# Kernel optimization log

Measured on AMD Instinct MI355X. Metric: run time of the kernel, lower is better.

## Reference

```python
import jax, jax.numpy as jnp
import numpy as np

NEG_SLOPE = 0.2


def _gat_layer(x, src, dst, W, att_src, att_dst, bias, concat):
    # x: [N, F_in]; W: [F_in, H*C]; att_*: [H, C]; bias: [H*C] or [C]
    N = x.shape[0]
    H, C = att_src.shape
    h = (x @ W).reshape(N, H, C)                      # [N, H, C]
    a_src = jnp.einsum('nhc,hc->nh', h, att_src)      # [N, H]
    a_dst = jnp.einsum('nhc,hc->nh', h, att_dst)      # [N, H]
    e = jax.nn.leaky_relu(a_src[src] + a_dst[dst], NEG_SLOPE)  # [E, H]
    # segment softmax over incoming edges of each destination node
    m = jax.ops.segment_max(e, dst, num_segments=N)   # [N, H]
    ex = jnp.exp(e - m[dst])
    s = jax.ops.segment_sum(ex, dst, num_segments=N)  # [N, H]
    alpha = ex / s[dst]                               # [E, H]
    out = jax.ops.segment_sum(h[src] * alpha[:, :, None], dst, num_segments=N)  # [N,H,C]
    out = out.reshape(N, H * C) if concat else out.mean(axis=1)
    return out + bias


def setup_inputs() -> dict:
    key = jax.random.key(0)
    ks = jax.random.split(key, 16)
    N, E, F = 50000, 1600000, 128
    HC1, H1 = 32, 4
    HC2, H2 = 32, 2
    NC, H3 = 2, 1     # layer3: 64 -> 2, 1 head, concat=False
    g = lambda k, shape, scale: jax.random.normal(k, shape, dtype=jnp.float32) * scale
    return {
        'x': g(ks[0], (N, F), 1.0),
        'edge_index': jax.random.randint(ks[1], (2, E), 0, N, dtype=jnp.int32),
        'W1': g(ks[2], (F, H1 * HC1), 0.1),
        'as1': g(ks[3], (H1, HC1), 0.1),
        'ad1': g(ks[4], (H1, HC1), 0.1),
        'b1': jnp.zeros((H1 * HC1,), jnp.float32),
        'W2': g(ks[5], (H1 * HC1, H2 * HC2), 0.1),
        'as2': g(ks[6], (H2, HC2), 0.1),
        'ad2': g(ks[7], (H2, HC2), 0.1),
        'b2': jnp.zeros((H2 * HC2,), jnp.float32),
        'W3': g(ks[8], (H2 * HC2, H3 * NC), 0.1),
        'as3': g(ks[9], (H3, NC), 0.1),
        'ad3': g(ks[10], (H3, NC), 0.1),
        'b3': jnp.zeros((NC,), jnp.float32),
    }


def reference(x, edge_index, W1, as1, ad1, b1, W2, as2, ad2, b2, W3, as3, ad3, b3):
    N = x.shape[0]
    # PyG GATConv adds self-loops by default
    loops = jnp.arange(N, dtype=edge_index.dtype)
    ei = jnp.concatenate([edge_index, jnp.stack([loops, loops])], axis=1)
    src, dst = ei[0], ei[1]
    h = _gat_layer(x, src, dst, W1, as1, ad1, b1, concat=True)
    h = jax.nn.elu(h)
    h = _gat_layer(h, src, dst, W2, as2, ad2, b2, concat=True)
    h = jax.nn.elu(h)
    h = _gat_layer(h, src, dst, W3, as3, ad3, b3, concat=False)
    return jax.nn.log_softmax(h, axis=1)
```

## Files before the change

kernel.cpp:

```cpp
#include <hip/hip_runtime.h>
#include <hip/hip_bf16.h>

#define NEG_SLOPE 0.2f
#define ARENA 10240

typedef __attribute__((ext_vector_type(8))) short short8v;
typedef __attribute__((ext_vector_type(4))) float f32x4;

__device__ __forceinline__ float bf_lo(uint32_t u) { return __uint_as_float(u << 16); }
__device__ __forceinline__ float bf_hi(uint32_t u) { return __uint_as_float(u & 0xffff0000u); }
__device__ __forceinline__ unsigned short f2bf(float f) {
    uint32_t u = __float_as_uint(f);
    u += 0x7fffu + ((u >> 16) & 1u);
    return (unsigned short)(u >> 16);
}
__device__ __forceinline__ float bf2f(unsigned short h) {
    return __uint_as_float((uint32_t)h << 16);
}

__device__ __forceinline__ int k_of(int l, int j) {
    return (l >> 4) * 4 + (j & 3) + 16 * (j >> 2);
}

template<int FIN, int FOUT>
__global__ void packW_kernel(const float* __restrict__ W, unsigned short* __restrict__ Wp) {
    constexpr int NT = FOUT / 16, KC = FIN / 32;
    int tid = blockIdx.x * blockDim.x + threadIdx.x;
    if (tid >= KC * NT * 64) return;
    int l  = tid & 63;
    int nt = (tid >> 6) % NT;
    int q  = tid / (64 * NT);
    int n  = nt * 16 + (l & 15);
    #pragma unroll
    for (int j = 0; j < 8; ++j) {
        int k = q * 32 + k_of(l, j);
        float v = W[k * FOUT + n];
        unsigned short h = f2bf(v);
        unsigned short lo = f2bf(v - bf2f(h));
        Wp[(((size_t)0 * KC + q) * NT + nt) * 512 + l * 8 + j] = h;
        Wp[(((size_t)1 * KC + q) * NT + nt) * 512 + l * 8 + j] = lo;
    }
}

template<int FIN, int FOUT, int H>
__global__ __launch_bounds__(256) void gemm_mfma_kernel(const float* __restrict__ X,
        const unsigned short* __restrict__ Wp, unsigned short* __restrict__ Hout,
        float* __restrict__ a_src, float* __restrict__ a_dst,
        const float* __restrict__ att_s, const float* __restrict__ att_d, int N) {
    constexpr int NT = FOUT / 16, KC = FIN / 32;
    __shared__ float sX[4][16 * FIN];
    int wv = threadIdx.x >> 6, l = threadIdx.x & 63;
    int mtile = blockIdx.x * 4 + wv;
    if (mtile * 16 >= N) return;
    const float* xsrc = X + (size_t)mtile * 16 * FIN;
    float* lds = sX[wv];
    #pragma unroll
    for (int i = 0; i < (16 * FIN) / 256; ++i) {
        int fi = (i * 64 + l) * 4;
        *(float4*)&lds[fi] = *(const float4*)&xsrc[fi];
    }
    __threadfence_block();

    int koff[8];
    #pragma unroll
    for (int j = 0; j < 8; ++j) koff[j] = k_of(l, j);
    int arow = (l & 15) * FIN;

    f32x4 acc[NT];
    #pragma unroll
    for (int nt = 0; nt < NT; ++nt) acc[nt] = f32x4{0.f, 0.f, 0.f, 0.f};

    const short8v* wp8 = (const short8v*)Wp;
    for (int q = 0; q < KC; ++q) {
        short8v ahi, alo;
        #pragma unroll
        for (int j = 0; j < 8; ++j) {
            float v = lds[arow + q * 32 + koff[j]];
            unsigned short h = f2bf(v);
            ahi[j] = (short)h;
            alo[j] = (short)f2bf(v - bf2f(h));
        }
        #pragma unroll
        for (int nt = 0; nt < NT; ++nt) {
            short8v bhi = wp8[((0 * KC + q) * NT + nt) * 64 + l];
            short8v blo = wp8[((1 * KC + q) * NT + nt) * 64 + l];
            acc[nt] = __builtin_amdgcn_mfma_f32_16x16x32_bf16(ahi, bhi, acc[nt], 0, 0, 0);
            acc[nt] = __builtin_amdgcn_mfma_f32_16x16x32_bf16(alo, bhi, acc[nt], 0, 0, 0);
            acc[nt] = __builtin_amdgcn_mfma_f32_16x16x32_bf16(ahi, blo, acc[nt], 0, 0, 0);
        }
    }

    constexpr int V = 4 * H;
    constexpr int PLOFF = 64 * V;
    float as_v[NT], ad_v[NT];
    #pragma unroll
    for (int nt = 0; nt < NT; ++nt) {
        as_v[nt] = att_s[nt * 16 + (l & 15)];
        ad_v[nt] = att_d[nt * 16 + (l & 15)];
    }
    float ps[4][H], pd[4][H];
    #pragma unroll
    for (int r = 0; r < 4; ++r)
        #pragma unroll
        for (int h = 0; h < H; ++h) { ps[r][h] = 0.f; pd[r][h] = 0.f; }
    #pragma unroll
    for (int nt = 0; nt < NT; ++nt)
        #pragma unroll
        for (int r = 0; r < 4; ++r) {
            ps[r][nt >> 1] += acc[nt][r] * as_v[nt];
            pd[r][nt >> 1] += acc[nt][r] * ad_v[nt];
        }
    float* sc = lds;
    int g = l >> 4, l16 = l & 15;
    int base = g * 16 * V + l16 * V;
    __threadfence_block();
    #pragma unroll
    for (int r = 0; r < 4; ++r)
        #pragma unroll
        for (int h = 0; h < H; ++h) {
            sc[base + r * H + h]         = ps[r][h];
            sc[PLOFF + base + r * H + h] = pd[r][h];
        }
    __threadfence_block();
    if (l16 < V) {
        float S = 0.f, D = 0.f;
        #pragma unroll
        for (int x = 0; x < 16; ++x) {
            S += sc[g * 16 * V + x * V + l16];
            D += sc[PLOFF + g * 16 * V + x * V + l16];
        }
        int r = l16 / H, h = l16 % H;
        int row = mtile * 16 + g * 4 + r;
        a_src[row * H + h] = S;
        a_dst[row * H + h] = D;
    }

    int row0 = mtile * 16 + (l >> 4) * 4;
    int col  = l & 15;
    #pragma unroll
    for (int nt = 0; nt < NT; ++nt)
        #pragma unroll
        for (int r = 0; r < 4; ++r)
            Hout[(size_t)(row0 + r) * FOUT + nt * 16 + col] = f2bf(acc[nt][r]);
}

template<int FIN, int FOUT, int H>
__global__ __launch_bounds__(256) void gemm_mfma_bf16_kernel(const unsigned short* __restrict__ X,
        const unsigned short* __restrict__ Wp, unsigned short* __restrict__ Hout,
        float* __restrict__ a_src, float* __restrict__ a_dst,
        const float* __restrict__ att_s, const float* __restrict__ att_d, int N) {
    constexpr int NT = FOUT / 16, KC = FIN / 32;
    constexpr int V = 4 * H;
    constexpr int PLOFF = 64 * V;
    __shared__ float sX[4][(16 * FIN) / 2 > 2 * PLOFF ? (16 * FIN) / 2 : 2 * PLOFF];
    int wv = threadIdx.x >> 6, l = threadIdx.x & 63;
    int mtile = blockIdx.x * 4 + wv;
    if (mtile * 16 >= N) return;
    const unsigned short* xsrc = X + (size_t)mtile * 16 * FIN;
    float* lds = sX[wv];
    unsigned short* ldsu = (unsigned short*)lds;
    #pragma unroll
    for (int i = 0; i < (16 * FIN) / 512; ++i) {
        int fi = (i * 64 + l) * 8;
        *(uint4*)&ldsu[fi] = *(const uint4*)&xsrc[fi];
    }
    __threadfence_block();

    int koff[8];
    #pragma unroll
    for (int j = 0; j < 8; ++j) koff[j] = k_of(l, j);
    int arow = (l & 15) * FIN;

    f32x4 acc[NT];
    #pragma unroll
    for (int nt = 0; nt < NT; ++nt) acc[nt] = f32x4{0.f, 0.f, 0.f, 0.f};

    const short8v* wp8 = (const short8v*)Wp;
    for (int q = 0; q < KC; ++q) {
        short8v ahi;
        #pragma unroll
        for (int j = 0; j < 8; ++j)
            ahi[j] = (short)ldsu[arow + q * 32 + koff[j]];
        #pragma unroll
        for (int nt = 0; nt < NT; ++nt) {
            short8v bhi = wp8[((0 * KC + q) * NT + nt) * 64 + l];
            short8v blo = wp8[((1 * KC + q) * NT + nt) * 64 + l];
            acc[nt] = __builtin_amdgcn_mfma_f32_16x16x32_bf16(ahi, bhi, acc[nt], 0, 0, 0);
            acc[nt] = __builtin_amdgcn_mfma_f32_16x16x32_bf16(ahi, blo, acc[nt], 0, 0, 0);
        }
    }

    float as_v[NT], ad_v[NT];
    #pragma unroll
    for (int nt = 0; nt < NT; ++nt) {
        as_v[nt] = att_s[nt * 16 + (l & 15)];
        ad_v[nt] = att_d[nt * 16 + (l & 15)];
    }
    float ps[4][H], pd[4][H];
    #pragma unroll
    for (int r = 0; r < 4; ++r)
        #pragma unroll
        for (int h = 0; h < H; ++h) { ps[r][h] = 0.f; pd[r][h] = 0.f; }
    #pragma unroll
    for (int nt = 0; nt < NT; ++nt)
        #pragma unroll
        for (int r = 0; r < 4; ++r) {
            ps[r][nt >> 1] += acc[nt][r] * as_v[nt];
            pd[r][nt >> 1] += acc[nt][r] * ad_v[nt];
        }
    float* sc = lds;
    int g = l >> 4, l16 = l & 15;
    int base = g * 16 * V + l16 * V;
    __threadfence_block();
    #pragma unroll
    for (int r = 0; r < 4; ++r)
        #pragma unroll
        for (int h = 0; h < H; ++h) {
            sc[base + r * H + h]         = ps[r][h];
            sc[PLOFF + base + r * H + h] = pd[r][h];
        }
    __threadfence_block();
    if (l16 < V) {
        float S = 0.f, D = 0.f;
        #pragma unroll
        for (int x = 0; x < 16; ++x) {
            S += sc[g * 16 * V + x * V + l16];
            D += sc[PLOFF + g * 16 * V + x * V + l16];
        }
        int r = l16 / H, h = l16 % H;
        int row = mtile * 16 + g * 4 + r;
        a_src[row * H + h] = S;
        a_dst[row * H + h] = D;
    }

    int row0 = mtile * 16 + (l >> 4) * 4;
    int col  = l & 15;
    #pragma unroll
    for (int nt = 0; nt < NT; ++nt)
        #pragma unroll
        for (int r = 0; r < 4; ++r)
            Hout[(size_t)(row0 + r) * FOUT + nt * 16 + col] = f2bf(acc[nt][r]);
}

__global__ void arena_init_kernel(int* __restrict__ bcur) {
    bcur[threadIdx.x] = threadIdx.x * ARENA;
}

__global__ __launch_bounds__(256) void bkt_scatter_kernel(const int* __restrict__ src,
        const int* __restrict__ dst, int* __restrict__ bcur,
        uint32_t* __restrict__ packed, int E) {
    __shared__ int lh[256], lbase[256], lcur[256];
    int tid = threadIdx.x;
    lh[tid] = 0; lcur[tid] = 0;
    __syncthreads();
    int chunk = (E + gridDim.x - 1) / gridDim.x;
    int e0 = blockIdx.x * chunk;
    int e1 = min(E, e0 + chunk);
    for (int e = e0 + tid; e < e1; e += 256)
        atomicAdd(&lh[dst[e] >> 8], 1);
    __syncthreads();
    if (lh[tid]) lbase[tid] = atomicAdd(&bcur[tid], lh[tid]);
    __syncthreads();
    for (int e = e0 + tid; e < e1; e += 256) {
        int d = dst[e];
        int b = d >> 8;
        int pos = lbase[b] + atomicAdd(&lcur[b], 1);
        packed[pos] = ((uint32_t)(d & 255) << 16) | (uint32_t)src[e];
    }
}

__global__ __launch_bounds__(256) void bkt_sort_kernel(const uint32_t* __restrict__ packed,
        const int* __restrict__ bcur, int* __restrict__ row_ptr, int* __restrict__ degA,
        unsigned short* __restrict__ colw, int N) {
    __shared__ int lh[256], lexcl[256], lcur[256];
    __shared__ int ws4[4];
    int tid = threadIdx.x, lane = tid & 63, wid = tid >> 6;
    int B = blockIdx.x;
    int seg0 = B * ARENA, seg1 = bcur[B];
    lh[tid] = 0; lcur[tid] = 0;
    __syncthreads();
    for (int i = seg0 + tid; i < seg1; i += 256)
        atomicAdd(&lh[packed[i] >> 16], 1);
    __syncthreads();
    int v = lh[tid];
    int x = v;
    #pragma unroll
    for (int off = 1; off < 64; off <<= 1) {
        int t = __shfl_up(x, off);
        if (lane >= off) x += t;
    }
    if (lane == 63) ws4[wid] = x;
    __syncthreads();
    int add = 0;
    #pragma unroll
    for (int w = 0; w < 4; ++w) if (w < wid) add += ws4[w];
    int excl = add + x - v;
    lexcl[tid] = excl;
    int d = B * 256 + tid;
    if (d < N) { row_ptr[d] = seg0 + excl; degA[d] = v; }
    __syncthreads();
    for (int i = seg0 + tid; i < seg1; i += 256) {
        uint32_t p = packed[i];
        int bin = p >> 16;
        int pos = seg0 + lexcl[bin] + atomicAdd(&lcur[bin], 1);
        colw[pos] = (unsigned short)(p & 0xFFFF);
    }
}

template<int H, int C, bool ELU, bool FUSE3>
__global__ __launch_bounds__(256) void agg_fused_kernel(
        const unsigned short* __restrict__ Hb, const float* __restrict__ a_src,
        const float* __restrict__ a_dst, const int* __restrict__ row_ptr,
        const int* __restrict__ degA, const unsigned short* __restrict__ colw,
        const float* __restrict__ bias, unsigned short* __restrict__ outb,
        const float* __restrict__ W3, const float* __restrict__ as3,
        const float* __restrict__ ad3, float* __restrict__ h3x4, int N) {
    constexpr int HC  = H * C;
    constexpr int LPW = HC / 4;
    constexpr int EPI = 64 / LPW;
    constexpr int SHIFT = (HC == 128) ? 8 : 7;
    static_assert(HC == 128 || HC == 64, "layout");
    __shared__ float sP[4][64 * H];
    __shared__ int   sS[4][64];
    int wv   = threadIdx.x >> 6;
    int lane = threadIdx.x & 63;
    int n = (int)(blockIdx.x * 4 + wv);
    if (n >= N) return;
    int start = row_ptr[n];
    int deg   = degA[n];

    float adv[H], cc[H], sp[H];
    #pragma unroll
    for (int h = 0; h < H; ++h) {
        adv[h] = a_dst[n * H + h];
        cc[h]  = fmaxf(adv[h], 0.f);
        sp[h]  = 0.f;
    }

    int sub = lane / LPW, pl = lane % LPW;
    int elem0 = pl * 4;
    int hh = elem0 / C;
    float a0 = 0.f, a1 = 0.f, a2 = 0.f, a3 = 0.f;

    for (int base = 0; base <= deg; base += 64) {
        int cnt = min(64, deg + 1 - base);
        int idx = base + lane;
        if (idx <= deg) {
            int srcn = (idx < deg) ? (int)colw[start + idx] : n;
            sS[wv][lane] = srcn;
            float av[H];
            if constexpr (H == 4) {
                float4 t = *(const float4*)&a_src[srcn * 4];
                av[0] = t.x; av[1] = t.y; av[2] = t.z; av[3] = t.w;
            } else {
                float2 t = *(const float2*)&a_src[srcn * 2];
                av[0] = t.x; av[1] = t.y;
            }
            #pragma unroll
            for (int h = 0; h < H; ++h) {
                float e = av[h] + adv[h];
                e = (e >= 0.f) ? e : NEG_SLOPE * e;
                float p = __expf(e - cc[h]);
                sp[h] += p;
                sP[wv][lane * H + h] = p;
            }
        }
        __threadfence_block();
        #pragma unroll 4
        for (int k = 0; k < cnt; k += EPI) {
            int eidx = k + sub;
            int eclm = min(eidx, cnt - 1);
            float w  = sP[wv][eclm * H + hh];
            int srcn = sS[wv][eclm];
            if (eidx >= cnt) w = 0.f;
            const char* pb = (const char*)Hb + (((size_t)srcn) << SHIFT) + elem0 * 2;
            uint2 pv = *(const uint2*)pb;
            a0 = fmaf(w, bf_lo(pv.x), a0);
            a1 = fmaf(w, bf_hi(pv.x), a1);
            a2 = fmaf(w, bf_lo(pv.y), a2);
            a3 = fmaf(w, bf_hi(pv.y), a3);
        }
        __threadfence_block();
    }

    #pragma unroll
    for (int off = 32; off; off >>= 1) {
        #pragma unroll
        for (int h = 0; h < H; ++h) sp[h] += __shfl_xor(sp[h], off);
    }
    #pragma unroll
    for (int off = 32; off >= LPW; off >>= 1) {
        a0 += __shfl_xor(a0, off); a1 += __shfl_xor(a1, off);
        a2 += __shfl_xor(a2, off); a3 += __shfl_xor(a3, off);
    }
    float inv = 1.f / sp[hh];
    float4 b4 = *(const float4*)&bias[elem0];
    float v0 = a0 * inv + b4.x, v1 = a1 * inv + b4.y;
    float v2 = a2 * inv + b4.z, v3 = a3 * inv + b4.w;
    if (ELU) {
        v0 = (v0 > 0.f) ? v0 : __expf(v0) - 1.f;
        v1 = (v1 > 0.f) ? v1 : __expf(v1) - 1.f;
        v2 = (v2 > 0.f) ? v2 : __expf(v2) - 1.f;
        v3 = (v3 > 0.f) ? v3 : __expf(v3) - 1.f;
    }
    if constexpr (!FUSE3) {
        if (sub == 0) {
            ushort4 o;
            o.x = f2bf(v0); o.y = f2bf(v1); o.z = f2bf(v2); o.w = f2bf(v3);
            *(ushort4*)&outb[(size_t)n * HC + elem0] = o;
        }
    } else {
        float p0 = v0 * W3[elem0 * 2]     + v1 * W3[elem0 * 2 + 2]
                 + v2 * W3[elem0 * 2 + 4] + v3 * W3[elem0 * 2 + 6];
        float p1 = v0 * W3[elem0 * 2 + 1] + v1 * W3[elem0 * 2 + 3]
                 + v2 * W3[elem0 * 2 + 5] + v3 * W3[elem0 * 2 + 7];
        #pragma unroll
        for (int off = 1; off < 16; off <<= 1) {
            p0 += __shfl_xor(p0, off);
            p1 += __shfl_xor(p1, off);
        }
        if (lane == 0) {
            float as = p0 * as3[0] + p1 * as3[1];
            float ad = p0 * ad3[0] + p1 * ad3[1];
            *(float4*)&h3x4[(size_t)n * 4] = make_float4(p0, p1, as, ad);
        }
    }
}

__global__ __launch_bounds__(256) void agg3_kernel(
        const float* __restrict__ h3x4, const int* __restrict__ row_ptr,
        const int* __restrict__ degA, const unsigned short* __restrict__ colw,
        const float* __restrict__ bias, float* __restrict__ out, int N) {
    int wave = (int)((blockIdx.x * blockDim.x + threadIdx.x) >> 6);
    int lane = threadIdx.x & 63;
    if (wave >= N) return;
    int n = wave;
    int start = row_ptr[n];
    int deg   = degA[n];
    float adv = h3x4[(size_t)n * 4 + 3];
    float c   = fmaxf(adv, 0.f);
    float s = 0.f, acc0 = 0.f, acc1 = 0.f;
    for (int i = lane; i <= deg; i += 64) {
        int srcn = (i < deg) ? (int)colw[start + i] : n;
        float4 g = *(const float4*)&h3x4[(size_t)srcn * 4];
        float e = g.z + adv;
        e = (e >= 0.f) ? e : NEG_SLOPE * e;
        float p = __expf(e - c);
        s += p;
        acc0 = fmaf(p, g.x, acc0);
        acc1 = fmaf(p, g.y, acc1);
    }
    #pragma unroll
    for (int off = 32; off; off >>= 1) {
        s    += __shfl_xor(s, off);
        acc0 += __shfl_xor(acc0, off);
        acc1 += __shfl_xor(acc1, off);
    }
    if (lane == 0) {
        float v0 = acc0 / s + bias[0];
        float v1 = acc1 / s + bias[1];
        float mx = fmaxf(v0, v1);
        float lse = mx + logf(__expf(v0 - mx) + __expf(v1 - mx));
        out[n * 2 + 0] = v0 - lse;
        out[n * 2 + 1] = v1 - lse;
    }
}

extern "C" void kernel_launch(void* const* d_in, const int* in_sizes, int n_in,
                              void* d_out, int out_size, void* d_ws, size_t ws_size,
                              hipStream_t stream) {
    const float* x   = (const float*)d_in[0];
    const int*   ei  = (const int*)d_in[1];
    const float* W1  = (const float*)d_in[2];
    const float* as1 = (const float*)d_in[3];
    const float* ad1 = (const float*)d_in[4];
    const float* b1  = (const float*)d_in[5];
    const float* W2  = (const float*)d_in[6];
    const float* as2 = (const float*)d_in[7];
    const float* ad2 = (const float*)d_in[8];
    const float* b2  = (const float*)d_in[9];
    const float* W3  = (const float*)d_in[10];
    const float* as3 = (const float*)d_in[11];
    const float* ad3 = (const float*)d_in[12];
    const float* b3  = (const float*)d_in[13];
    int N = in_sizes[0] / 128;
    int E = in_sizes[1] / 2;
    const int* src = ei;
    const int* dst = ei + E;
    int NB = (N + 255) / 256;

    char* ws = (char*)d_ws;
    size_t off = 0;
    auto alloc = [&](size_t bytes) -> void* {
        void* p = ws + off;
        off = (off + bytes + 255) & ~(size_t)255;
        return p;
    };
    int*            bcur    = (int*)alloc(256 * 4);
    int*            row_ptr = (int*)alloc((size_t)N * 4);
    int*            degA    = (int*)alloc((size_t)N * 4);
    uint32_t*       packed  = (uint32_t*)alloc((size_t)NB * ARENA * 4);
    unsigned short* colw    = (unsigned short*)alloc((size_t)NB * ARENA * 2);
    unsigned short* hb      = (unsigned short*)alloc((size_t)N * 128 * 2);
    unsigned short* obuf    = (unsigned short*)alloc((size_t)N * 128 * 2);
    float*          h3x4    = (float*)alloc((size_t)N * 4 * 4);
    float*          asrc    = (float*)alloc((size_t)N * 4 * 4);
    float*          adst    = (float*)alloc((size_t)N * 4 * 4);
    unsigned short* Wp1     = (unsigned short*)alloc((size_t)2 * 4 * 8 * 512 * 2);
    unsigned short* Wp2     = (unsigned short*)alloc((size_t)2 * 4 * 4 * 512 * 2);

    packW_kernel<128, 128><<<8, 256, 0, stream>>>(W1, Wp1);
    packW_kernel<128, 64><<<4, 256, 0, stream>>>(W2, Wp2);

    arena_init_kernel<<<1, 256, 0, stream>>>(bcur);
    bkt_scatter_kernel<<<256, 256, 0, stream>>>(src, dst, bcur, packed, E);
    bkt_sort_kernel<<<NB, 256, 0, stream>>>(packed, bcur, row_ptr, degA, colw, N);

    int gmblocks = ((N + 15) / 16 + 3) / 4;

    gemm_mfma_kernel<128, 128, 4><<<gmblocks, 256, 0, stream>>>(x, Wp1, hb, asrc, adst, as1, ad1, N);
    agg_fused_kernel<4, 32, true, false><<<(N + 3) / 4, 256, 0, stream>>>(
        hb, asrc, adst, row_ptr, degA, colw, b1, obuf, nullptr, nullptr, nullptr, nullptr, N);

    gemm_mfma_bf16_kernel<128, 64, 2><<<gmblocks, 256, 0, stream>>>(obuf, Wp2, hb, asrc, adst, as2, ad2, N);
    agg_fused_kernel<2, 32, true, true><<<(N + 3) / 4, 256, 0, stream>>>(
        hb, asrc, adst, row_ptr, degA, colw, b2, nullptr, W3, as3, ad3, h3x4, N);

    agg3_kernel<<<(N + 3) / 4, 256, 0, stream>>>(h3x4, row_ptr, degA, colw, b3, (float*)d_out, N);
}
```

Measured before the change: 197.9 us.

## Split layer-1 aggregation into per-head phases for cache locality

```diff
diff --git a/kernel.cpp b/kernel.cpp
--- a/kernel.cpp
+++ b/kernel.cpp
@@ -307,19 +307,101 @@
     }
 }
 
-template<int H, int C, bool ELU, bool FUSE3>
-__global__ __launch_bounds__(256) void agg_fused_kernel(
+template<int H, int C>
+__global__ __launch_bounds__(256) void agg_sliced_kernel(
         const unsigned short* __restrict__ Hb, const float* __restrict__ a_src,
         const float* __restrict__ a_dst, const int* __restrict__ row_ptr,
         const int* __restrict__ degA, const unsigned short* __restrict__ colw,
         const float* __restrict__ bias, unsigned short* __restrict__ outb,
-        const float* __restrict__ W3, const float* __restrict__ as3,
-        const float* __restrict__ ad3, float* __restrict__ h3x4, int N) {
+        int BPH, int N) {
+    constexpr int HC   = H * C;
+    constexpr int LPW  = C / 4;
+    constexpr int EPI  = 64 / LPW;
+    constexpr int SHIFT = (HC == 128) ? 8 : 7;
+    __shared__ float sP[4][64];
+    __shared__ int   sS[4][64];
+    int wv   = threadIdx.x >> 6;
+    int lane = threadIdx.x & 63;
+    int hphase = blockIdx.x / BPH;
+    int nb     = blockIdx.x % BPH;
+    int n = nb * 4 + wv;
+    if (n >= N) return;
+    int start = row_ptr[n];
+    int deg   = degA[n];
+
+    float adv = a_dst[n * H + hphase];
+    float cc  = fmaxf(adv, 0.f);
+    float sp  = 0.f;
+
+    int sub = lane / LPW, pl = lane % LPW;
+    uint32_t boff = (uint32_t)((hphase * C + pl * 4) * 2);
+    float a0 = 0.f, a1 = 0.f, a2 = 0.f, a3 = 0.f;
+
+    for (int base = 0; base <= deg; base += 64) {
+        int cnt = min(64, deg + 1 - base);
+        int idx = base + lane;
+        if (idx <= deg) {
+            int srcn = (idx < deg) ? (int)colw[start + idx] : n;
+            sS[wv][lane] = srcn;
+            float e = a_src[srcn * H + hphase] + adv;
+            e = (e >= 0.f) ? e : NEG_SLOPE * e;
+            float p = __expf(e - cc);
+            sp += p;
+            sP[wv][lane] = p;
+        }
+        __threadfence_block();
+        #pragma unroll 2
+        for (int k = 0; k < cnt; k += EPI) {
+            int eidx = k + sub;
+            int eclm = min(eidx, cnt - 1);
+            float w  = sP[wv][eclm];
+            int srcn = sS[wv][eclm];
+            if (eidx >= cnt) w = 0.f;
+            const char* pb = (const char*)Hb + (((size_t)srcn) << SHIFT) + boff;
+            uint2 pv = *(const uint2*)pb;
+            a0 = fmaf(w, bf_lo(pv.x), a0);
+            a1 = fmaf(w, bf_hi(pv.x), a1);
+            a2 = fmaf(w, bf_lo(pv.y), a2);
+            a3 = fmaf(w, bf_hi(pv.y), a3);
+        }
+        __threadfence_block();
+    }
+
+    #pragma unroll
+    for (int off = 32; off; off >>= 1) sp += __shfl_xor(sp, off);
+    #pragma unroll
+    for (int off = 32; off >= LPW; off >>= 1) {
+        a0 += __shfl_xor(a0, off); a1 += __shfl_xor(a1, off);
+        a2 += __shfl_xor(a2, off); a3 += __shfl_xor(a3, off);
+    }
+    if (sub == 0) {
+        int e0 = hphase * C + pl * 4;
+        float inv = 1.f / sp;
+        float4 b4 = *(const float4*)&bias[e0];
+        float v0 = a0 * inv + b4.x, v1 = a1 * inv + b4.y;
+        float v2 = a2 * inv + b4.z, v3 = a3 * inv + b4.w;
+        v0 = (v0 > 0.f) ? v0 : __expf(v0) - 1.f;
+        v1 = (v1 > 0.f) ? v1 : __expf(v1) - 1.f;
+        v2 = (v2 > 0.f) ? v2 : __expf(v2) - 1.f;
+        v3 = (v3 > 0.f) ? v3 : __expf(v3) - 1.f;
+        ushort4 o;
+        o.x = f2bf(v0); o.y = f2bf(v1); o.z = f2bf(v2); o.w = f2bf(v3);
+        *(ushort4*)&outb[(size_t)n * HC + e0] = o;
+    }
+}
+
+template<int H, int C>
+__global__ __launch_bounds__(256) void agg_fused3_kernel(
+        const unsigned short* __restrict__ Hb, const float* __restrict__ a_src,
+        const float* __restrict__ a_dst, const int* __restrict__ row_ptr,
+        const int* __restrict__ degA, const unsigned short* __restrict__ colw,
+        const float* __restrict__ bias, const float* __restrict__ W3,
+        const float* __restrict__ as3, const float* __restrict__ ad3,
+        float* __restrict__ h3x4, int N) {
     constexpr int HC  = H * C;
     constexpr int LPW = HC / 4;
     constexpr int EPI = 64 / LPW;
     constexpr int SHIFT = (HC == 128) ? 8 : 7;
-    static_assert(HC == 128 || HC == 64, "layout");
     __shared__ float sP[4][64 * H];
     __shared__ int   sS[4][64];
     int wv   = threadIdx.x >> 6;
@@ -348,14 +430,8 @@
         if (idx <= deg) {
             int srcn = (idx < deg) ? (int)colw[start + idx] : n;
             sS[wv][lane] = srcn;
-            float av[H];
-            if constexpr (H == 4) {
-                float4 t = *(const float4*)&a_src[srcn * 4];
-                av[0] = t.x; av[1] = t.y; av[2] = t.z; av[3] = t.w;
-            } else {
-                float2 t = *(const float2*)&a_src[srcn * 2];
-                av[0] = t.x; av[1] = t.y;
-            }
+            float2 t = *(const float2*)&a_src[srcn * 2];
+            float av[2] = {t.x, t.y};
             #pragma unroll
             for (int h = 0; h < H; ++h) {
                 float e = av[h] + adv[h];
@@ -397,33 +473,23 @@
     float4 b4 = *(const float4*)&bias[elem0];
     float v0 = a0 * inv + b4.x, v1 = a1 * inv + b4.y;
     float v2 = a2 * inv + b4.z, v3 = a3 * inv + b4.w;
-    if (ELU) {
-        v0 = (v0 > 0.f) ? v0 : __expf(v0) - 1.f;
-        v1 = (v1 > 0.f) ? v1 : __expf(v1) - 1.f;
-        v2 = (v2 > 0.f) ? v2 : __expf(v2) - 1.f;
-        v3 = (v3 > 0.f) ? v3 : __expf(v3) - 1.f;
-    }
-    if constexpr (!FUSE3) {
-        if (sub == 0) {
-            ushort4 o;
-            o.x = f2bf(v0); o.y = f2bf(v1); o.z = f2bf(v2); o.w = f2bf(v3);
-            *(ushort4*)&outb[(size_t)n * HC + elem0] = o;
-        }
-    } else {
-        float p0 = v0 * W3[elem0 * 2]     + v1 * W3[elem0 * 2 + 2]
-                 + v2 * W3[elem0 * 2 + 4] + v3 * W3[elem0 * 2 + 6];
-        float p1 = v0 * W3[elem0 * 2 + 1] + v1 * W3[elem0 * 2 + 3]
-                 + v2 * W3[elem0 * 2 + 5] + v3 * W3[elem0 * 2 + 7];
-        #pragma unroll
-        for (int off = 1; off < 16; off <<= 1) {
-            p0 += __shfl_xor(p0, off);
-            p1 += __shfl_xor(p1, off);
-        }
-        if (lane == 0) {
-            float as = p0 * as3[0] + p1 * as3[1];
-            float ad = p0 * ad3[0] + p1 * ad3[1];
-            *(float4*)&h3x4[(size_t)n * 4] = make_float4(p0, p1, as, ad);
-        }
+    v0 = (v0 > 0.f) ? v0 : __expf(v0) - 1.f;
+    v1 = (v1 > 0.f) ? v1 : __expf(v1) - 1.f;
+    v2 = (v2 > 0.f) ? v2 : __expf(v2) - 1.f;
+    v3 = (v3 > 0.f) ? v3 : __expf(v3) - 1.f;
+    float p0 = v0 * W3[elem0 * 2]     + v1 * W3[elem0 * 2 + 2]
+             + v2 * W3[elem0 * 2 + 4] + v3 * W3[elem0 * 2 + 6];
+    float p1 = v0 * W3[elem0 * 2 + 1] + v1 * W3[elem0 * 2 + 3]
+             + v2 * W3[elem0 * 2 + 5] + v3 * W3[elem0 * 2 + 7];
+    #pragma unroll
+    for (int off = 1; off < 16; off <<= 1) {
+        p0 += __shfl_xor(p0, off);
+        p1 += __shfl_xor(p1, off);
+    }
+    if (lane == 0) {
+        float as = p0 * as3[0] + p1 * as3[1];
+        float ad = p0 * ad3[0] + p1 * ad3[1];
+        *(float4*)&h3x4[(size_t)n * 4] = make_float4(p0, p1, as, ad);
     }
 }
 
@@ -517,14 +583,15 @@
     bkt_sort_kernel<<<NB, 256, 0, stream>>>(packed, bcur, row_ptr, degA, colw, N);
 
     int gmblocks = ((N + 15) / 16 + 3) / 4;
+    int BPH = (N + 3) / 4;
 
     gemm_mfma_kernel<128, 128, 4><<<gmblocks, 256, 0, stream>>>(x, Wp1, hb, asrc, adst, as1, ad1, N);
-    agg_fused_kernel<4, 32, true, false><<<(N + 3) / 4, 256, 0, stream>>>(
-        hb, asrc, adst, row_ptr, degA, colw, b1, obuf, nullptr, nullptr, nullptr, nullptr, N);
+    agg_sliced_kernel<4, 32><<<4 * BPH, 256, 0, stream>>>(
+        hb, asrc, adst, row_ptr, degA, colw, b1, obuf, BPH, N);
 
     gemm_mfma_bf16_kernel<128, 64, 2><<<gmblocks, 256, 0, stream>>>(obuf, Wp2, hb, asrc, adst, as2, ad2, N);
-    agg_fused_kernel<2, 32, true, true><<<(N + 3) / 4, 256, 0, stream>>>(
-        hb, asrc, adst, row_ptr, degA, colw, b2, nullptr, W3, as3, ad3, h3x4, N);
+    agg_fused3_kernel<2, 32><<<(N + 3) / 4, 256, 0, stream>>>(
+        hb, asrc, adst, row_ptr, degA, colw, b2, W3, as3, ad3, h3x4, N);
 
     agg3_kernel<<<(N + 3) / 4, 256, 0, stream>>>(h3x4, row_ptr, degA, colw, b3, (float*)d_out, N);
 }
```

Measured after the change: 249.6 us. 1.26x slower.
